# Kernel optimization log

Hardware: AMD Instinct MI355X
Metric: run time of the kernel (lower is better)

Reference implementation:

```python
import jax, jax.numpy as jnp
import numpy as np
from jax import lax

B, T, H, OUT = 2048, 512, 128, 64  # batch, lookback, hidden, horizon


def _p(k, shape):
    return jax.random.normal(k, shape, jnp.float32) * 0.1


def setup_inputs() -> dict:
    key = jax.random.key(0)
    ks = jax.random.split(key, 19)
    d = {"x": jax.random.normal(ks[0], (B, T), jnp.float32)}
    i = 1
    for pre in ("enc", "dec"):
        for l in range(2):
            insz = 1 if l == 0 else H
            d[f"{pre}_Wih{l}"] = _p(ks[i], (4 * H, insz)); i += 1
            d[f"{pre}_Whh{l}"] = _p(ks[i], (4 * H, H)); i += 1
            d[f"{pre}_bih{l}"] = _p(ks[i], (4 * H,)); i += 1
            d[f"{pre}_bhh{l}"] = _p(ks[i], (4 * H,)); i += 1
    d["lin_W"] = _p(ks[17], (1, H))
    d["lin_b"] = _p(ks[18], (1,))
    return d


def _cell(x, h, c, Wih, Whh, bih, bhh):
    # PyTorch LSTM gate order: i, f, g, o
    gates = x @ Wih.T + h @ Whh.T + bih + bhh  # [B, 4H]
    i, f, g, o = jnp.split(gates, 4, axis=-1)
    c = jax.nn.sigmoid(f) * c + jax.nn.sigmoid(i) * jnp.tanh(g)
    h = jax.nn.sigmoid(o) * jnp.tanh(c)
    return h, c


def _layer(xs, Wih, Whh, bih, bhh):
    # xs: [T, B, in] -> (ys [T, B, H], final (h, c))
    b = xs.shape[1]
    h0 = jnp.zeros((b, Whh.shape[1]), xs.dtype)
    def step(carry, x):
        h, c = _cell(x, carry[0], carry[1], Wih, Whh, bih, bhh)
        return (h, c), h
    (h, c), ys = lax.scan(step, (h0, h0), xs)
    return ys, (h, c)


def reference(x,
              enc_Wih0, enc_Whh0, enc_bih0, enc_bhh0,
              enc_Wih1, enc_Whh1, enc_bih1, enc_bhh1,
              dec_Wih0, dec_Whh0, dec_bih0, dec_bhh0,
              dec_Wih1, dec_Whh1, dec_bih1, dec_bhh1,
              lin_W, lin_b):
    xs = x.T[:, :, None]  # [T, B, 1]
    ys0, (h0, c0) = _layer(xs, enc_Wih0, enc_Whh0, enc_bih0, enc_bhh0)
    _,   (h1, c1) = _layer(ys0, enc_Wih1, enc_Whh1, enc_bih1, enc_bhh1)

    inp0 = x[:, -1:]  # [B, 1] last observed price
    def dec_step(carry, _):
        inp, a, b_, h, c = carry
        a, b_ = _cell(inp, a, b_, dec_Wih0, dec_Whh0, dec_bih0, dec_bhh0)
        h, c = _cell(a, h, c, dec_Wih1, dec_Whh1, dec_bih1, dec_bhh1)
        pred = h @ lin_W.T + lin_b  # [B, 1]
        return (pred, a, b_, h, c), pred[:, 0]

    _, preds = lax.scan(dec_step, (inp0, h0, c0, h1, c1), None, length=OUT)
    return preds.T  # [B, OUT]
```

## Files before the change

### kernel.cpp

```cpp
#include <hip/hip_runtime.h>


typedef _Float16 half_t;
typedef _Float16 f16x8 __attribute__((ext_vector_type(8)));
typedef float    f32x4 __attribute__((ext_vector_type(4)));

#define BT   8
#define H    128
#define T    512
#define OUTS 64

__device__ __forceinline__ float sigm(float x)   { return 1.0f / (1.0f + __expf(-x)); }
__device__ __forceinline__ float tanh_f(float x) { return 2.0f / (1.0f + __expf(-2.0f * x)) - 1.0f; }

__device__ __forceinline__ void mfma_a(f32x4& d, f16x8 a, const f16x8& b) {
  asm("v_mfma_f32_16x16x32_f16 %0, %1, %2, %0" : "+v"(d) : "v"(a), "a"(b));
}
__device__ __forceinline__ void mfma_v(f32x4& d, f16x8 a, const f16x8& b) {
  asm("v_mfma_f32_16x16x32_f16 %0, %1, %2, %0" : "+v"(d) : "v"(a), "v"(b));
}
__device__ __forceinline__ void mfma_aa(f32x4& d, f16x8 a, const f16x8& b) {
  asm("v_mfma_f32_16x16x32_f16 %0, %1, %2, %0" : "+a"(d) : "v"(a), "a"(b));
}

__device__ __forceinline__ f16x8 lda(const half_t* buf, int col, int kg, int kb) {
  int b  = col >> 1;
  int bc = (kb * 64 + kg * 16) ^ (b << 4);
  return *(const f16x8*)((const char*)buf + b * 256 + bc);
}

__device__ __forceinline__ void wr_h(half_t* hb, int b, int j, float h) {
  int bc = (j * 2) ^ (b << 4);
  *(half_t*)((char*)hb + b * 256 + bc) = (half_t)h;
}

template <int M>
__device__ __forceinline__ void pass_a(f32x4 (&acc)[2][4], const f16x8 (&wa)[2][4][2][4],
                                       const half_t* buf, int col, int kg) {
#pragma unroll
  for (int kb = 0; kb < 4; kb++) {
    f16x8 a = lda(buf, col, kg, kb);
#pragma unroll
    for (int jt = 0; jt < 2; jt++)
#pragma unroll
      for (int q = 0; q < 4; q++)
        mfma_a(acc[jt][q], a, wa[M][q][jt][kb]);
  }
}

__device__ __forceinline__ void pass_v(f32x4 (&acc)[2][4], const f16x8 (&wv2)[4][2][4],
                                       const half_t* buf, int col, int kg) {
#pragma unroll
  for (int kb = 0; kb < 4; kb++) {
    f16x8 a = lda(buf, col, kg, kb);
#pragma unroll
    for (int jt = 0; jt < 2; jt++)
#pragma unroll
      for (int q = 0; q < 4; q++)
        mfma_v(acc[jt][q], a, wv2[q][jt][kb]);
  }
}

__device__ __forceinline__ void zacc(f32x4 (&acc)[2][4]) {
#pragma unroll
  for (int jt = 0; jt < 2; jt++)
#pragma unroll
    for (int q = 0; q < 4; q++) acc[jt][q] = (f32x4){0.f, 0.f, 0.f, 0.f};
}

__device__ __forceinline__ void load_wa(f16x8 (&wa)[2][4][2][4], const half_t* w16,
                                        int base, int wv, int col, int kg) {
#pragma unroll
  for (int m = 0; m < 2; m++)
#pragma unroll
    for (int q = 0; q < 4; q++)
#pragma unroll
      for (int jt = 0; jt < 2; jt++)
#pragma unroll
        for (int kb = 0; kb < 4; kb++) {
          wa[m][q][jt][kb] = *(const f16x8*)(w16 + (size_t)(base + m) * 65536 +
                                             (size_t)(q * 128 + wv * 32 + jt * 16 + col) * 128 +
                                             kb * 32 + kg * 8);
          asm("" : "+a"(wa[m][q][jt][kb]));
        }
}

__device__ __forceinline__ void load_wv(f16x8 (&wv2)[4][2][4], const half_t* w16,
                                        int base, int wv, int col, int kg) {
#pragma unroll
  for (int q = 0; q < 4; q++)
#pragma unroll
    for (int jt = 0; jt < 2; jt++)
#pragma unroll
      for (int kb = 0; kb < 4; kb++)
        wv2[q][jt][kb] = *(const f16x8*)(w16 + (size_t)(base + 2) * 65536 +
                                         (size_t)(q * 128 + wv * 32 + jt * 16 + col) * 128 +
                                         kb * 32 + kg * 8);
}

template <int M>
__device__ __forceinline__ void pass8(f32x4 (&acc)[4], const f16x8 (&wa)[3][4][4],
                                      const half_t* buf, int col, int kg) {
#pragma unroll
  for (int kb = 0; kb < 4; kb++) {
    f16x8 a = lda(buf, col, kg, kb);
#pragma unroll
    for (int q = 0; q < 4; q++)
      mfma_aa(acc[q], a, wa[M][q][kb]);
  }
}

__device__ __forceinline__ void zacc8(f32x4 (&acc)[4]) {
#pragma unroll
  for (int q = 0; q < 4; q++) acc[q] = (f32x4){0.f, 0.f, 0.f, 0.f};
}

__device__ __forceinline__ void load_w8(f16x8 (&wa)[3][4][4], const half_t* w16,
                                        int base, int wv, int col, int kg) {
#pragma unroll
  for (int m = 0; m < 3; m++)
#pragma unroll
    for (int q = 0; q < 4; q++) {
#pragma unroll
      for (int kb = 0; kb < 4; kb++) {
        wa[m][q][kb] = *(const f16x8*)(w16 + (size_t)(base + m) * 65536 +
                                       (size_t)(q * 128 + wv * 16 + col) * 128 +
                                       kb * 32 + kg * 8);
        asm("" : "+a"(wa[m][q][kb]));
      }
      asm volatile("s_waitcnt vmcnt(0)" ::: "memory");
    }
}

__global__ void prep_kernel(const float* m0, const float* m1, const float* m2,
                            const float* m3, const float* m4, const float* m5,
                            const float* ba0, const float* bb0, const float* ba1, const float* bb1,
                            const float* ba2, const float* bb2, const float* ba3, const float* bb3,
                            const float* encWih0, const float* decWih0,
                            half_t* w16, float* biasT, float* xwT) {
  int i = blockIdx.x * 256 + threadIdx.x;
  if (i < 6 * 65536) {
    int m = i >> 16, e = i & 65535;
    const float* src = (m == 0) ? m0 : (m == 1) ? m1 : (m == 2) ? m2
                     : (m == 3) ? m3 : (m == 4) ? m4 : m5;
    w16[i] = (half_t)src[e];
  }
  if (i < 2048) {
    int set = i >> 9, wi = i & 511, q = wi >> 7, jh = wi & 127;
    const float* A  = (set == 0) ? ba0 : (set == 1) ? ba1 : (set == 2) ? ba2 : ba3;
    const float* Bv = (set == 0) ? bb0 : (set == 1) ? bb1 : (set == 2) ? bb2 : bb3;
    biasT[set * 512 + jh * 4 + q] = A[wi] + Bv[wi];
  }
  if (i < 1024) {
    int ph = i >> 9, wi = i & 511, q = wi >> 7, jh = wi & 127;
    xwT[ph * 512 + jh * 4 + q] = (ph ? decWih0 : encWih0)[wi];
  }
}

__global__ __launch_bounds__(256, 1)
void lstm_all(const float* __restrict__ x, const float* __restrict__ linW,
              const float* __restrict__ linb, const half_t* __restrict__ w16,
              const float* __restrict__ biasTg, const float* __restrict__ xwTg,
              float* __restrict__ out)
{
  __shared__ alignas(16) half_t h0b[2][BT * H];
  __shared__ alignas(16) half_t h1b[2][BT * H];
  __shared__ float xch[64 * BT];
  __shared__ float h1f[BT * H];
  __shared__ float linWs[H];
  __shared__ float pp[256];
  __shared__ float predbuf[BT];

  const int tid  = threadIdx.x;
  const int wv   = tid >> 6;
  const int lane = tid & 63;
  const int col  = lane & 15;
  const int kg   = lane >> 4;
  const int b0   = blockIdx.x * BT;

  for (int z = tid; z < 1024; z += 256) {
    ((unsigned*)h0b)[z] = 0u; ((unsigned*)h1b)[z] = 0u;
  }
  if (tid < H) linWs[tid] = linW[tid];

  f16x8 wa[2][4][2][4];
  f16x8 wv2[4][2][4];
  load_wa(wa, w16, 0, wv, col, kg);
  load_wv(wv2, w16, 0, wv, col, kg);

  float b0r[2][4], b1r[2][4], xwr[2][4];
#pragma unroll
  for (int jt = 0; jt < 2; jt++) {
    const int jj = wv * 32 + jt * 16 + col;
#pragma unroll
    for (int q = 0; q < 4; q++) {
      b0r[jt][q] = biasTg[jj * 4 + q];
      b1r[jt][q] = biasTg[512 + jj * 4 + q];
      xwr[jt][q] = xwTg[jj * 4 + q];
    }
  }

  float c0[2][2] = {{0, 0}, {0, 0}};
  float c1[2][2] = {{0, 0}, {0, 0}};

  for (int e = tid; e < BT * 64; e += 256) {
    int b = e >> 6, j = e & 63;
    xch[j * 8 + b] = x[(size_t)(b0 + b) * T + j];
  }
  __syncthreads();

  {
    f32x4 acc[2][4];
    zacc(acc);
    pass_a<0>(acc, wa, h0b[0], col, kg);
#pragma unroll
    for (int jt = 0; jt < 2; jt++) {
      const int jj = wv * 32 + jt * 16 + col;
#pragma unroll
      for (int s = 0; s < 2; s++) {
        const int b = 2 * kg + s;
        const int e = 2 * s;
        float xv = xch[0 * 8 + b];
        float gi = acc[jt][0][e] + b0r[jt][0] + xv * xwr[jt][0];
        float gf = acc[jt][1][e] + b0r[jt][1] + xv * xwr[jt][1];
        float gg = acc[jt][2][e] + b0r[jt][2] + xv * xwr[jt][2];
        float go = acc[jt][3][e] + b0r[jt][3] + xv * xwr[jt][3];
        float cn = sigm(gf) * c0[jt][s] + sigm(gi) * tanh_f(gg);
        c0[jt][s] = cn;
        wr_h(h0b[1], b, jj, sigm(go) * tanh_f(cn));
      }
    }
  }
  __syncthreads();
  int p = 1;

  for (int S = 0; S < 511; S++) {
    if (((S + 1) & 63) == 0) {
      const int ch = (S + 1) >> 6;
      for (int e = tid; e < BT * 64; e += 256) {
        int b = e >> 6, j = e & 63;
        xch[j * 8 + b] = x[(size_t)(b0 + b) * T + ch * 64 + j];
      }
      __syncthreads();
    }
    const int np = p ^ 1;
    f32x4 acc[2][4];
    zacc(acc);
    pass_v(acc, wv2, h1b[p], col, kg);
    pass_a<1>(acc, wa, h0b[p], col, kg);
#pragma unroll
    for (int jt = 0; jt < 2; jt++) {
      const int jj = wv * 32 + jt * 16 + col;
#pragma unroll
      for (int s = 0; s < 2; s++) {
        const int b = 2 * kg + s;
        const int e = 2 * s;
        float gi = acc[jt][0][e] + b1r[jt][0];
        float gf = acc[jt][1][e] + b1r[jt][1];
        float gg = acc[jt][2][e] + b1r[jt][2];
        float go = acc[jt][3][e] + b1r[jt][3];
        float cn = sigm(gf) * c1[jt][s] + sigm(gi) * tanh_f(gg);
        c1[jt][s] = cn;
        wr_h(h1b[np], b, jj, sigm(go) * tanh_f(cn));
      }
    }
    zacc(acc);
    pass_a<0>(acc, wa, h0b[p], col, kg);
#pragma unroll
    for (int jt = 0; jt < 2; jt++) {
      const int jj = wv * 32 + jt * 16 + col;
#pragma unroll
      for (int s = 0; s < 2; s++) {
        const int b = 2 * kg + s;
        const int e = 2 * s;
        float xv = xch[((S + 1) & 63) * 8 + b];
        float gi = acc[jt][0][e] + b0r[jt][0] + xv * xwr[jt][0];
        float gf = acc[jt][1][e] + b0r[jt][1] + xv * xwr[jt][1];
        float gg = acc[jt][2][e] + b0r[jt][2] + xv * xwr[jt][2];
        float go = acc[jt][3][e] + b0r[jt][3] + xv * xwr[jt][3];
        float cn = sigm(gf) * c0[jt][s] + sigm(gi) * tanh_f(gg);
        c0[jt][s] = cn;
        wr_h(h0b[np], b, jj, sigm(go) * tanh_f(cn));
      }
    }
    __syncthreads();
    p = np;
  }

  {
    const int np = p ^ 1;
    f32x4 acc[2][4];
    zacc(acc);
    pass_v(acc, wv2, h1b[p], col, kg);
    pass_a<1>(acc, wa, h0b[p], col, kg);
#pragma unroll
    for (int jt = 0; jt < 2; jt++) {
      const int jj = wv * 32 + jt * 16 + col;
#pragma unroll
      for (int s = 0; s < 2; s++) {
        const int b = 2 * kg + s;
        const int e = 2 * s;
        float gi = acc[jt][0][e] + b1r[jt][0];
        float gf = acc[jt][1][e] + b1r[jt][1];
        float gg = acc[jt][2][e] + b1r[jt][2];
        float go = acc[jt][3][e] + b1r[jt][3];
        float cn = sigm(gf) * c1[jt][s] + sigm(gi) * tanh_f(gg);
        c1[jt][s] = cn;
        wr_h(h1b[np], b, jj, sigm(go) * tanh_f(cn));
      }
    }
    __syncthreads();
  }
  int p0 = p;
  int p1 = p ^ 1;

  load_wa(wa, w16, 3, wv, col, kg);
  load_wv(wv2, w16, 3, wv, col, kg);
#pragma unroll
  for (int jt = 0; jt < 2; jt++) {
    const int jj = wv * 32 + jt * 16 + col;
#pragma unroll
    for (int q = 0; q < 4; q++) {
      b0r[jt][q] = biasTg[1024 + jj * 4 + q];
      b1r[jt][q] = biasTg[1536 + jj * 4 + q];
      xwr[jt][q] = xwTg[512 + jj * 4 + q];
    }
  }
  const float lb = linb[0];
  if (tid < BT) predbuf[tid] = x[(size_t)(b0 + tid) * T + (T - 1)];
  __syncthreads();

  for (int so = 0; so < OUTS; so++) {
    const int n0 = p0 ^ 1, n1 = p1 ^ 1;
    f32x4 acc[2][4];
    zacc(acc);
    pass_a<0>(acc, wa, h0b[p0], col, kg);
#pragma unroll
    for (int jt = 0; jt < 2; jt++) {
      const int jj = wv * 32 + jt * 16 + col;
#pragma unroll
      for (int s = 0; s < 2; s++) {
        const int b = 2 * kg + s;
        const int e = 2 * s;
        float xv = predbuf[b];
        float gi = acc[jt][0][e] + b0r[jt][0] + xv * xwr[jt][0];
        float gf = acc[jt][1][e] + b0r[jt][1] + xv * xwr[jt][1];
        float gg = acc[jt][2][e] + b0r[jt][2] + xv * xwr[jt][2];
        float go = acc[jt][3][e] + b0r[jt][3] + xv * xwr[jt][3];
        float cn = sigm(gf) * c0[jt][s] + sigm(gi) * tanh_f(gg);
        c0[jt][s] = cn;
        wr_h(h0b[n0], b, jj, sigm(go) * tanh_f(cn));
      }
    }
    __syncthreads();
    zacc(acc);
    pass_v(acc, wv2, h1b[p1], col, kg);
    pass_a<1>(acc, wa, h0b[n0], col, kg);
#pragma unroll
    for (int jt = 0; jt < 2; jt++) {
      const int jj = wv * 32 + jt * 16 + col;
#pragma unroll
      for (int s = 0; s < 2; s++) {
        const int b = 2 * kg + s;
        const int e = 2 * s;
        float cn = sigm(acc[jt][1][e] + b1r[jt][1]) * c1[jt][s]
                 + sigm(acc[jt][0][e] + b1r[jt][0]) * tanh_f(acc[jt][2][e] + b1r[jt][2]);
        c1[jt][s] = cn;
        float hn = sigm(acc[jt][3][e] + b1r[jt][3]) * tanh_f(cn);
        wr_h(h1b[n1], b, jj, hn);
        h1f[b * H + jj] = hn;
      }
    }
    __syncthreads();
    {
      int r = tid >> 5, seg = tid & 31;
      float pv = 0.0f;
#pragma unroll
      for (int kk = 0; kk < 4; kk++) pv += h1f[r * H + seg * 4 + kk] * linWs[seg * 4 + kk];
      pp[tid] = pv;
    }
    __syncthreads();
    if (tid < BT) {
      float pv = lb;
#pragma unroll
      for (int g2 = 0; g2 < 32; g2++) pv += pp[tid * 32 + g2];
      predbuf[tid] = pv;
      out[(size_t)(b0 + tid) * OUTS + so] = pv;
    }
    __syncthreads();
    p0 = n0; p1 = n1;
  }
}

__global__ __launch_bounds__(512, 2)
void lstm_all8(const float* __restrict__ x, const float* __restrict__ linW,
               const float* __restrict__ linb, const half_t* __restrict__ w16,
               const float* __restrict__ biasTg, const float* __restrict__ xwTg,
               float* __restrict__ out)
{
  __shared__ alignas(16) half_t h0b[2][BT * H];
  __shared__ alignas(16) half_t h1b[2][BT * H];
  __shared__ float xch[64 * BT];
  __shared__ float h1f[BT * H];
  __shared__ float linWs[H];
  __shared__ float pp[256];
  __shared__ float predbuf[BT];

  const int tid  = threadIdx.x;
  const int wv   = tid >> 6;
  const int lane = tid & 63;
  const int col  = lane & 15;
  const int kg   = lane >> 4;
  const int b0   = blockIdx.x * BT;

  for (int z = tid; z < 1024; z += 512) {
    ((unsigned*)h0b)[z] = 0u; ((unsigned*)h1b)[z] = 0u;
  }
  if (tid < H) linWs[tid] = linW[tid];

  f16x8 wa[3][4][4];
  load_w8(wa, w16, 0, wv, col, kg);

  float b0r[4], b1r[4], xwr[4];
  {
    const int jj = wv * 16 + col;
#pragma unroll
    for (int q = 0; q < 4; q++) {
      b0r[q] = biasTg[jj * 4 + q];
      b1r[q] = biasTg[512 + jj * 4 + q];
      xwr[q] = xwTg[jj * 4 + q];
    }
  }

  float c0[2] = {0, 0};
  float c1[2] = {0, 0};

  for (int e = tid; e < BT * 64; e += 512) {
    int b = e >> 6, j = e & 63;
    xch[j * 8 + b] = x[(size_t)(b0 + b) * T + j];
  }
  __syncthreads();

  {
    f32x4 acc[4];
    zacc8(acc);
    pass8<0>(acc, wa, h0b[0], col, kg);
    const int jj = wv * 16 + col;
#pragma unroll
    for (int s = 0; s < 2; s++) {
      const int b = 2 * kg + s;
      const int e = 2 * s;
      float xv = xch[0 * 8 + b];
      float gi = acc[0][e] + b0r[0] + xv * xwr[0];
      float gf = acc[1][e] + b0r[1] + xv * xwr[1];
      float gg = acc[2][e] + b0r[2] + xv * xwr[2];
      float go = acc[3][e] + b0r[3] + xv * xwr[3];
      float cn = sigm(gf) * c0[s] + sigm(gi) * tanh_f(gg);
      c0[s] = cn;
      wr_h(h0b[1], b, jj, sigm(go) * tanh_f(cn));
    }
  }
  __syncthreads();
  int p = 1;

  for (int S = 0; S < 511; S++) {
    if (((S + 1) & 63) == 0) {
      const int ch = (S + 1) >> 6;
      for (int e = tid; e < BT * 64; e += 512) {
        int b = e >> 6, j = e & 63;
        xch[j * 8 + b] = x[(size_t)(b0 + b) * T + ch * 64 + j];
      }
      __syncthreads();
    }
    const int np = p ^ 1;
    f32x4 acc[4];
    zacc8(acc);
    pass8<2>(acc, wa, h1b[p], col, kg);
    pass8<1>(acc, wa, h0b[p], col, kg);
    {
      const int jj = wv * 16 + col;
#pragma unroll
      for (int s = 0; s < 2; s++) {
        const int b = 2 * kg + s;
        const int e = 2 * s;
        float gi = acc[0][e] + b1r[0];
        float gf = acc[1][e] + b1r[1];
        float gg = acc[2][e] + b1r[2];
        float go = acc[3][e] + b1r[3];
        float cn = sigm(gf) * c1[s] + sigm(gi) * tanh_f(gg);
        c1[s] = cn;
        wr_h(h1b[np], b, jj, sigm(go) * tanh_f(cn));
      }
    }
    zacc8(acc);
    pass8<0>(acc, wa, h0b[p], col, kg);
    {
      const int jj = wv * 16 + col;
#pragma unroll
      for (int s = 0; s < 2; s++) {
        const int b = 2 * kg + s;
        const int e = 2 * s;
        float xv = xch[((S + 1) & 63) * 8 + b];
        float gi = acc[0][e] + b0r[0] + xv * xwr[0];
        float gf = acc[1][e] + b0r[1] + xv * xwr[1];
        float gg = acc[2][e] + b0r[2] + xv * xwr[2];
        float go = acc[3][e] + b0r[3] + xv * xwr[3];
        float cn = sigm(gf) * c0[s] + sigm(gi) * tanh_f(gg);
        c0[s] = cn;
        wr_h(h0b[np], b, jj, sigm(go) * tanh_f(cn));
      }
    }
    __syncthreads();
    p = np;
  }

  {
    const int np = p ^ 1;
    f32x4 acc[4];
    zacc8(acc);
    pass8<2>(acc, wa, h1b[p], col, kg);
    pass8<1>(acc, wa, h0b[p], col, kg);
    const int jj = wv * 16 + col;
#pragma unroll
    for (int s = 0; s < 2; s++) {
      const int b = 2 * kg + s;
      const int e = 2 * s;
      float gi = acc[0][e] + b1r[0];
      float gf = acc[1][e] + b1r[1];
      float gg = acc[2][e] + b1r[2];
      float go = acc[3][e] + b1r[3];
      float cn = sigm(gf) * c1[s] + sigm(gi) * tanh_f(gg);
      c1[s] = cn;
      wr_h(h1b[np], b, jj, sigm(go) * tanh_f(cn));
    }
    __syncthreads();
  }
  int p0 = p;
  int p1 = p ^ 1;

  load_w8(wa, w16, 3, wv, col, kg);
  {
    const int jj = wv * 16 + col;
#pragma unroll
    for (int q = 0; q < 4; q++) {
      b0r[q] = biasTg[1024 + jj * 4 + q];
      b1r[q] = biasTg[1536 + jj * 4 + q];
      xwr[q] = xwTg[512 + jj * 4 + q];
    }
  }
  const float lb = linb[0];
  if (tid < BT) predbuf[tid] = x[(size_t)(b0 + tid) * T + (T - 1)];
  __syncthreads();

  for (int so = 0; so < OUTS; so++) {
    const int n0 = p0 ^ 1, n1 = p1 ^ 1;
    f32x4 acc[4];
    zacc8(acc);
    pass8<0>(acc, wa, h0b[p0], col, kg);
    {
      const int jj = wv * 16 + col;
#pragma unroll
      for (int s = 0; s < 2; s++) {
        const int b = 2 * kg + s;
        const int e = 2 * s;
        float xv = predbuf[b];
        float gi = acc[0][e] + b0r[0] + xv * xwr[0];
        float gf = acc[1][e] + b0r[1] + xv * xwr[1];
        float gg = acc[2][e] + b0r[2] + xv * xwr[2];
        float go = acc[3][e] + b0r[3] + xv * xwr[3];
        float cn = sigm(gf) * c0[s] + sigm(gi) * tanh_f(gg);
        c0[s] = cn;
        wr_h(h0b[n0], b, jj, sigm(go) * tanh_f(cn));
      }
    }
    __syncthreads();
    zacc8(acc);
    pass8<2>(acc, wa, h1b[p1], col, kg);
    pass8<1>(acc, wa, h0b[n0], col, kg);
    {
      const int jj = wv * 16 + col;
#pragma unroll
      for (int s = 0; s < 2; s++) {
        const int b = 2 * kg + s;
        const int e = 2 * s;
        float cn = sigm(acc[1][e] + b1r[1]) * c1[s]
                 + sigm(acc[0][e] + b1r[0]) * tanh_f(acc[2][e] + b1r[2]);
        c1[s] = cn;
        float hn = sigm(acc[3][e] + b1r[3]) * tanh_f(cn);
        wr_h(h1b[n1], b, jj, hn);
        h1f[b * H + jj] = hn;
      }
    }
    __syncthreads();
    if (tid < 256) {
      int r = tid >> 5, seg = tid & 31;
      float pv = 0.0f;
#pragma unroll
      for (int kk = 0; kk < 4; kk++) pv += h1f[r * H + seg * 4 + kk] * linWs[seg * 4 + kk];
      pp[tid] = pv;
    }
    __syncthreads();
    if (tid < BT) {
      float pv = lb;
#pragma unroll
      for (int g2 = 0; g2 < 32; g2++) pv += pp[tid * 32 + g2];
      predbuf[tid] = pv;
      out[(size_t)(b0 + tid) * OUTS + so] = pv;
    }
    __syncthreads();
    p0 = n0; p1 = n1;
  }
}

extern "C" void kernel_launch(void* const* d_in, const int* in_sizes, int n_in,
                              void* d_out, int out_size, void* d_ws, size_t ws_size,
                              hipStream_t stream) {
  const float* x        = (const float*)d_in[0];
  const float* encWih0  = (const float*)d_in[1];
  const float* encWhh0  = (const float*)d_in[2];
  const float* encbih0  = (const float*)d_in[3];
  const float* encbhh0  = (const float*)d_in[4];
  const float* encWih1  = (const float*)d_in[5];
  const float* encWhh1  = (const float*)d_in[6];
  const float* encbih1  = (const float*)d_in[7];
  const float* encbhh1  = (const float*)d_in[8];
  const float* decWih0  = (const float*)d_in[9];
  const float* decWhh0  = (const float*)d_in[10];
  const float* decbih0  = (const float*)d_in[11];
  const float* decbhh0  = (const float*)d_in[12];
  const float* decWih1  = (const float*)d_in[13];
  const float* decWhh1  = (const float*)d_in[14];
  const float* decbih1  = (const float*)d_in[15];
  const float* decbhh1  = (const float*)d_in[16];
  const float* linW     = (const float*)d_in[17];
  const float* linb     = (const float*)d_in[18];

  half_t* w16  = (half_t*)d_ws;
  float*  biasT = (float*)((char*)d_ws + (size_t)6 * 65536 * 2);
  float*  xwT   = biasT + 2048;

  prep_kernel<<<1536, 256, 0, stream>>>(encWhh0, encWih1, encWhh1, decWhh0, decWih1, decWhh1,
                                        encbih0, encbhh0, encbih1, encbhh1,
                                        decbih0, decbhh0, decbih1, decbhh1,
                                        encWih0, decWih0, w16, biasT, xwT);

  static int use8 = -1;
  if (use8 < 0) {
    hipFuncAttributes attr{};
    int occ = 0;
    hipError_t e1 = hipFuncGetAttributes(&attr, (const void*)lstm_all8);
    hipError_t e2 = hipOccupancyMaxActiveBlocksPerMultiprocessor(&occ, (const void*)lstm_all8,
                                                                 512, 0);
    use8 = (e1 == hipSuccess && e2 == hipSuccess && occ >= 1 && attr.localSizeBytes == 0) ? 1 : 0;
  }
  if (use8)
    lstm_all8<<<256, 512, 0, stream>>>(x, linW, linb, w16, biasT, xwT, (float*)d_out);
  else
    lstm_all<<<256, 256, 0, stream>>>(x, linW, linb, w16, biasT, xwT, (float*)d_out);
}
```

Measured before the change: 1.312 ms.

## Move one weight matrix from AGPRs into LDS to cut register pressure

The kernel keeps two of its three recurrent weight matrices (layer-0 Whh and layer-1 Wih) in AGPRs and stages the third, the layer-1 Whh, into 128 KB of dynamic LDS. MFMA B-operands for that matrix are now read from LDS each step. Accumulators move from AGPRs to VGPRs. This frees registers, at the cost of extra LDS traffic on every step. The large LDS footprint allows only one 512-thread block per CU, and the host falls back to the older kernel if the dynamic shared memory attribute or the occupancy query fails.

After: 1.315 ms. No clear change (+0.3%).

```diff
diff --git a/kernel.cpp b/kernel.cpp
--- a/kernel.cpp
+++ b/kernel.cpp
@@ -18,9 +18,6 @@
 }
 __device__ __forceinline__ void mfma_v(f32x4& d, f16x8 a, const f16x8& b) {
   asm("v_mfma_f32_16x16x32_f16 %0, %1, %2, %0" : "+v"(d) : "v"(a), "v"(b));
-}
-__device__ __forceinline__ void mfma_aa(f32x4& d, f16x8 a, const f16x8& b) {
-  asm("v_mfma_f32_16x16x32_f16 %0, %1, %2, %0" : "+a"(d) : "v"(a), "a"(b));
 }
 
 __device__ __forceinline__ f16x8 lda(const half_t* buf, int col, int kg, int kb) {
@@ -99,14 +96,27 @@
 }
 
 template <int M>
-__device__ __forceinline__ void pass8(f32x4 (&acc)[4], const f16x8 (&wa)[3][4][4],
-                                      const half_t* buf, int col, int kg) {
+__device__ __forceinline__ void pass_g(f32x4 (&acc)[4], const f16x8 (&wa)[2][4][4],
+                                       const half_t* buf, int col, int kg) {
 #pragma unroll
   for (int kb = 0; kb < 4; kb++) {
     f16x8 a = lda(buf, col, kg, kb);
 #pragma unroll
     for (int q = 0; q < 4; q++)
-      mfma_aa(acc[q], a, wa[M][q][kb]);
+      mfma_a(acc[q], a, wa[M][q][kb]);
+  }
+}
+
+__device__ __forceinline__ void pass_l(f32x4 (&acc)[4], const half_t* wldsw,
+                                       const half_t* buf, int col, int kg, int lane) {
+#pragma unroll
+  for (int kb = 0; kb < 4; kb++) {
+    f16x8 a = lda(buf, col, kg, kb);
+#pragma unroll
+    for (int q = 0; q < 4; q++) {
+      f16x8 bf = *(const f16x8*)(wldsw + (q * 4 + kb) * 512 + lane * 8);
+      mfma_v(acc[q], a, bf);
+    }
   }
 }
 
@@ -115,10 +125,10 @@
   for (int q = 0; q < 4; q++) acc[q] = (f32x4){0.f, 0.f, 0.f, 0.f};
 }
 
-__device__ __forceinline__ void load_w8(f16x8 (&wa)[3][4][4], const half_t* w16,
+__device__ __forceinline__ void load_w2(f16x8 (&wa)[2][4][4], const half_t* w16,
                                         int base, int wv, int col, int kg) {
 #pragma unroll
-  for (int m = 0; m < 3; m++)
+  for (int m = 0; m < 2; m++)
 #pragma unroll
     for (int q = 0; q < 4; q++) {
 #pragma unroll
@@ -130,6 +140,21 @@
       }
       asm volatile("s_waitcnt vmcnt(0)" ::: "memory");
     }
+}
+
+__device__ __forceinline__ void stage_wlds(half_t* wldsw, const half_t* w16, int slot,
+                                           int wv, int col, int kg, int lane) {
+#pragma unroll
+  for (int q = 0; q < 4; q++) {
+#pragma unroll
+    for (int kb = 0; kb < 4; kb++) {
+      f16x8 v = *(const f16x8*)(w16 + (size_t)slot * 65536 +
+                                (size_t)(q * 128 + wv * 16 + col) * 128 +
+                                kb * 32 + kg * 8);
+      *(f16x8*)(wldsw + (q * 4 + kb) * 512 + lane * 8) = v;
+    }
+    asm volatile("s_waitcnt vmcnt(0)" ::: "memory");
+  }
 }
 
 __global__ void prep_kernel(const float* m0, const float* m1, const float* m2,
@@ -393,18 +418,22 @@
 }
 
 __global__ __launch_bounds__(512, 2)
-void lstm_all8(const float* __restrict__ x, const float* __restrict__ linW,
-               const float* __restrict__ linb, const half_t* __restrict__ w16,
-               const float* __restrict__ biasTg, const float* __restrict__ xwTg,
-               float* __restrict__ out)
+void lstm_lds(const float* __restrict__ x, const float* __restrict__ linW,
+              const float* __restrict__ linb, const half_t* __restrict__ w16,
+              const float* __restrict__ biasTg, const float* __restrict__ xwTg,
+              float* __restrict__ out)
 {
-  __shared__ alignas(16) half_t h0b[2][BT * H];
-  __shared__ alignas(16) half_t h1b[2][BT * H];
-  __shared__ float xch[64 * BT];
-  __shared__ float h1f[BT * H];
-  __shared__ float linWs[H];
-  __shared__ float pp[256];
-  __shared__ float predbuf[BT];
+  extern __shared__ char dyn[];
+  half_t* wlds   = (half_t*)dyn;
+  half_t* h0b0   = (half_t*)(dyn + 131072);
+  half_t* h0b1   = (half_t*)(dyn + 133120);
+  half_t* h1b0   = (half_t*)(dyn + 135168);
+  half_t* h1b1   = (half_t*)(dyn + 137216);
+  float*  xch    = (float*)(dyn + 139264);
+  float*  h1f    = (float*)(dyn + 141312);
+  float*  linWs  = (float*)(dyn + 145408);
+  float*  pp     = (float*)(dyn + 145920);
+  float*  predbuf= (float*)(dyn + 146944);
 
   const int tid  = threadIdx.x;
   const int wv   = tid >> 6;
@@ -412,18 +441,19 @@
   const int col  = lane & 15;
   const int kg   = lane >> 4;
   const int b0   = blockIdx.x * BT;
-
-  for (int z = tid; z < 1024; z += 512) {
-    ((unsigned*)h0b)[z] = 0u; ((unsigned*)h1b)[z] = 0u;
-  }
+  half_t* wldsw  = wlds + wv * 8192;
+
+  for (int z = tid; z < 2048; z += 512)
+    ((unsigned*)(dyn + 131072))[z] = 0u;
   if (tid < H) linWs[tid] = linW[tid];
 
-  f16x8 wa[3][4][4];
-  load_w8(wa, w16, 0, wv, col, kg);
+  f16x8 wa[2][4][4];
+  load_w2(wa, w16, 0, wv, col, kg);
+  stage_wlds(wldsw, w16, 2, wv, col, kg, lane);
 
   float b0r[4], b1r[4], xwr[4];
+  const int jj = wv * 16 + col;
   {
-    const int jj = wv * 16 + col;
 #pragma unroll
     for (int q = 0; q < 4; q++) {
       b0r[q] = biasTg[jj * 4 + q];
@@ -444,8 +474,7 @@
   {
     f32x4 acc[4];
     zacc8(acc);
-    pass8<0>(acc, wa, h0b[0], col, kg);
-    const int jj = wv * 16 + col;
+    pass_g<0>(acc, wa, h0b0, col, kg);
 #pragma unroll
     for (int s = 0; s < 2; s++) {
       const int b = 2 * kg + s;
@@ -457,7 +486,7 @@
       float go = acc[3][e] + b0r[3] + xv * xwr[3];
       float cn = sigm(gf) * c0[s] + sigm(gi) * tanh_f(gg);
       c0[s] = cn;
-      wr_h(h0b[1], b, jj, sigm(go) * tanh_f(cn));
+      wr_h(h0b1, b, jj, sigm(go) * tanh_f(cn));
     }
   }
   __syncthreads();
@@ -473,54 +502,14 @@
       __syncthreads();
     }
     const int np = p ^ 1;
+    half_t* h0p = p ? h0b1 : h0b0;
+    half_t* h0n = p ? h0b0 : h0b1;
+    half_t* h1p = p ? h1b1 : h1b0;
+    half_t* h1n = p ? h1b0 : h1b1;
     f32x4 acc[4];
     zacc8(acc);
-    pass8<2>(acc, wa, h1b[p], col, kg);
-    pass8<1>(acc, wa, h0b[p], col, kg);
-    {
-      const int jj = wv * 16 + col;
-#pragma unroll
-      for (int s = 0; s < 2; s++) {
-        const int b = 2 * kg + s;
-        const int e = 2 * s;
-        float gi = acc[0][e] + b1r[0];
-        float gf = acc[1][e] + b1r[1];
-        float gg = acc[2][e] + b1r[2];
-        float go = acc[3][e] + b1r[3];
-        float cn = sigm(gf) * c1[s] + sigm(gi) * tanh_f(gg);
-        c1[s] = cn;
-        wr_h(h1b[np], b, jj, sigm(go) * tanh_f(cn));
-      }
-    }
-    zacc8(acc);
-    pass8<0>(acc, wa, h0b[p], col, kg);
-    {
-      const int jj = wv * 16 + col;
-#pragma unroll
-      for (int s = 0; s < 2; s++) {
-        const int b = 2 * kg + s;
-        const int e = 2 * s;
-        float xv = xch[((S + 1) & 63) * 8 + b];
-        float gi = acc[0][e] + b0r[0] + xv * xwr[0];
-        float gf = acc[1][e] + b0r[1] + xv * xwr[1];
-        float gg = acc[2][e] + b0r[2] + xv * xwr[2];
-        float go = acc[3][e] + b0r[3] + xv * xwr[3];
-        float cn = sigm(gf) * c0[s] + sigm(gi) * tanh_f(gg);
-        c0[s] = cn;
-        wr_h(h0b[np], b, jj, sigm(go) * tanh_f(cn));
-      }
-    }
-    __syncthreads();
-    p = np;
-  }
-
-  {
-    const int np = p ^ 1;
-    f32x4 acc[4];
-    zacc8(acc);
-    pass8<2>(acc, wa, h1b[p], col, kg);
-    pass8<1>(acc, wa, h0b[p], col, kg);
-    const int jj = wv * 16 + col;
+    pass_l(acc, wldsw, h1p, col, kg, lane);
+    pass_g<1>(acc, wa, h0p, col, kg);
 #pragma unroll
     for (int s = 0; s < 2; s++) {
       const int b = 2 * kg + s;
@@ -531,16 +520,57 @@
       float go = acc[3][e] + b1r[3];
       float cn = sigm(gf) * c1[s] + sigm(gi) * tanh_f(gg);
       c1[s] = cn;
-      wr_h(h1b[np], b, jj, sigm(go) * tanh_f(cn));
-    }
-    __syncthreads();
+      wr_h(h1n, b, jj, sigm(go) * tanh_f(cn));
+    }
+    zacc8(acc);
+    pass_g<0>(acc, wa, h0p, col, kg);
+#pragma unroll
+    for (int s = 0; s < 2; s++) {
+      const int b = 2 * kg + s;
+      const int e = 2 * s;
+      float xv = xch[((S + 1) & 63) * 8 + b];
+      float gi = acc[0][e] + b0r[0] + xv * xwr[0];
+      float gf = acc[1][e] + b0r[1] + xv * xwr[1];
+      float gg = acc[2][e] + b0r[2] + xv * xwr[2];
+      float go = acc[3][e] + b0r[3] + xv * xwr[3];
+      float cn = sigm(gf) * c0[s] + sigm(gi) * tanh_f(gg);
+      c0[s] = cn;
+      wr_h(h0n, b, jj, sigm(go) * tanh_f(cn));
+    }
+    __syncthreads();
+    p = np;
+  }
+
+  {
+    const int np = p ^ 1;
+    half_t* h0p = p ? h0b1 : h0b0;
+    half_t* h1p = p ? h1b1 : h1b0;
+    half_t* h1n = p ? h1b0 : h1b1;
+    f32x4 acc[4];
+    zacc8(acc);
+    pass_l(acc, wldsw, h1p, col, kg, lane);
+    pass_g<1>(acc, wa, h0p, col, kg);
+#pragma unroll
+    for (int s = 0; s < 2; s++) {
+      const int b = 2 * kg + s;
+      const int e = 2 * s;
+      float gi = acc[0][e] + b1r[0];
+      float gf = acc[1][e] + b1r[1];
+      float gg = acc[2][e] + b1r[2];
+      float go = acc[3][e] + b1r[3];
+      float cn = sigm(gf) * c1[s] + sigm(gi) * tanh_f(gg);
+      c1[s] = cn;
+      wr_h(h1n, b, jj, sigm(go) * tanh_f(cn));
+    }
+    __syncthreads();
+    (void)np;
   }
   int p0 = p;
   int p1 = p ^ 1;
 
-  load_w8(wa, w16, 3, wv, col, kg);
+  load_w2(wa, w16, 3, wv, col, kg);
+  stage_wlds(wldsw, w16, 5, wv, col, kg, lane);
   {
-    const int jj = wv * 16 + col;
 #pragma unroll
     for (int q = 0; q < 4; q++) {
       b0r[q] = biasTg[1024 + jj * 4 + q];
@@ -554,42 +584,40 @@
 
   for (int so = 0; so < OUTS; so++) {
     const int n0 = p0 ^ 1, n1 = p1 ^ 1;
+    half_t* h0p = p0 ? h0b1 : h0b0;
+    half_t* h0n = p0 ? h0b0 : h0b1;
+    half_t* h1p = p1 ? h1b1 : h1b0;
+    half_t* h1n = p1 ? h1b0 : h1b1;
     f32x4 acc[4];
     zacc8(acc);
-    pass8<0>(acc, wa, h0b[p0], col, kg);
-    {
-      const int jj = wv * 16 + col;
-#pragma unroll
-      for (int s = 0; s < 2; s++) {
-        const int b = 2 * kg + s;
-        const int e = 2 * s;
-        float xv = predbuf[b];
-        float gi = acc[0][e] + b0r[0] + xv * xwr[0];
-        float gf = acc[1][e] + b0r[1] + xv * xwr[1];
-        float gg = acc[2][e] + b0r[2] + xv * xwr[2];
-        float go = acc[3][e] + b0r[3] + xv * xwr[3];
-        float cn = sigm(gf) * c0[s] + sigm(gi) * tanh_f(gg);
-        c0[s] = cn;
-        wr_h(h0b[n0], b, jj, sigm(go) * tanh_f(cn));
-      }
+    pass_g<0>(acc, wa, h0p, col, kg);
+#pragma unroll
+    for (int s = 0; s < 2; s++) {
+      const int b = 2 * kg + s;
+      const int e = 2 * s;
+      float xv = predbuf[b];
+      float gi = acc[0][e] + b0r[0] + xv * xwr[0];
+      float gf = acc[1][e] + b0r[1] + xv * xwr[1];
+      float gg = acc[2][e] + b0r[2] + xv * xwr[2];
+      float go = acc[3][e] + b0r[3] + xv * xwr[3];
+      float cn = sigm(gf) * c0[s] + sigm(gi) * tanh_f(gg);
+      c0[s] = cn;
+      wr_h(h0n, b, jj, sigm(go) * tanh_f(cn));
     }
     __syncthreads();
     zacc8(acc);
-    pass8<2>(acc, wa, h1b[p1], col, kg);
-    pass8<1>(acc, wa, h0b[n0], col, kg);
-    {
-      const int jj = wv * 16 + col;
-#pragma unroll
-      for (int s = 0; s < 2; s++) {
-        const int b = 2 * kg + s;
-        const int e = 2 * s;
-        float cn = sigm(acc[1][e] + b1r[1]) * c1[s]
-                 + sigm(acc[0][e] + b1r[0]) * tanh_f(acc[2][e] + b1r[2]);
-        c1[s] = cn;
-        float hn = sigm(acc[3][e] + b1r[3]) * tanh_f(cn);
-        wr_h(h1b[n1], b, jj, hn);
-        h1f[b * H + jj] = hn;
-      }
+    pass_l(acc, wldsw, h1p, col, kg, lane);
+    pass_g<1>(acc, wa, h0n, col, kg);
+#pragma unroll
+    for (int s = 0; s < 2; s++) {
+      const int b = 2 * kg + s;
+      const int e = 2 * s;
+      float cn = sigm(acc[1][e] + b1r[1]) * c1[s]
+               + sigm(acc[0][e] + b1r[0]) * tanh_f(acc[2][e] + b1r[2]);
+      c1[s] = cn;
+      float hn = sigm(acc[3][e] + b1r[3]) * tanh_f(cn);
+      wr_h(h1n, b, jj, hn);
+      h1f[b * H + jj] = hn;
     }
     __syncthreads();
     if (tid < 256) {
@@ -644,17 +672,20 @@
                                         decbih0, decbhh0, decbih1, decbhh1,
                                         encWih0, decWih0, w16, biasT, xwT);
 
-  static int use8 = -1;
-  if (use8 < 0) {
+  static int useL = -1;
+  if (useL < 0) {
+    hipError_t e0 = hipFuncSetAttribute((const void*)lstm_lds,
+                                        hipFuncAttributeMaxDynamicSharedMemorySize, 147456);
     hipFuncAttributes attr{};
     int occ = 0;
-    hipError_t e1 = hipFuncGetAttributes(&attr, (const void*)lstm_all8);
-    hipError_t e2 = hipOccupancyMaxActiveBlocksPerMultiprocessor(&occ, (const void*)lstm_all8,
-                                                                 512, 0);
-    use8 = (e1 == hipSuccess && e2 == hipSuccess && occ >= 1 && attr.localSizeBytes == 0) ? 1 : 0;
-  }
-  if (use8)
-    lstm_all8<<<256, 512, 0, stream>>>(x, linW, linb, w16, biasT, xwT, (float*)d_out);
+    hipError_t e1 = hipFuncGetAttributes(&attr, (const void*)lstm_lds);
+    hipError_t e2 = hipOccupancyMaxActiveBlocksPerMultiprocessor(&occ, (const void*)lstm_lds,
+                                                                 512, 147456);
+    useL = (e0 == hipSuccess && e1 == hipSuccess && e2 == hipSuccess &&
+            occ >= 1 && attr.localSizeBytes == 0) ? 1 : 0;
+  }
+  if (useL)
+    lstm_lds<<<256, 512, 147456, stream>>>(x, linW, linb, w16, biasT, xwT, (float*)d_out);
   else
     lstm_all<<<256, 256, 0, stream>>>(x, linW, linb, w16, biasT, xwT, (float*)d_out);
 }
```
